# Kernel tuning notes

Hardware: AMD Instinct MI355X
Metric: run time of the kernel (lower is better)

## Reference

```python
import jax, jax.numpy as jnp
import numpy as np

EPS = 1e-8  # torch cosine_similarity default eps


def setup_inputs() -> dict:
    key = jax.random.key(0)
    x = jax.random.normal(key, (256, 200, 1024), dtype=jnp.float32)
    return {"x": x}


def reference(x):
    # x: [B, c, l]
    # Cosine-similarity Gram matrix, fused: dot(i,j) / max(||x_i||*||x_j||, eps)
    norms = jnp.linalg.norm(x, axis=-1)                      # [B, c]
    dots = jnp.einsum('bil,bjl->bij', x, x)                  # [B, c, c]
    sim = dots / jnp.maximum(norms[:, :, None] * norms[:, None, :], EPS)
    atten = jax.nn.softmax(sim, axis=-1)                     # [B, c, c]
    out = jnp.einsum('bij,bjl->bil', atten, x) + x           # bmm + residual
    return out
```

## Files before the change

kernel.cpp:

```cpp
#include <hip/hip_runtime.h>
#include <math.h>


typedef unsigned int uint32;
typedef __attribute__((ext_vector_type(8))) short bf16x8;
typedef __attribute__((ext_vector_type(4))) float f32x4;

#define CC 200
#define LL 1024
#define EPSV 1e-8f
#define PLSTR 116
#define XASTR 36
#define TSTR 116

__device__ __forceinline__ uint32 bfb(float f) {
  uint32 u = __float_as_uint(f);
  u += 0x7fffu + ((u >> 16) & 1u);
  return u >> 16;
}

__global__ __launch_bounds__(512, 1)
void spe_attn_kernel(const float* __restrict__ x, float* __restrict__ out) {
  const int tid  = threadIdx.x;
  const int lane = tid & 63;
  const int w    = tid >> 6;
  const int lm   = lane & 15;
  const int lg   = lane >> 4;
  const int bidx = blockIdx.x;
  const float* xb = x + (size_t)bidx * (CC * LL);
  float* ob       = out + (size_t)bidx * (CC * LL);

  __shared__ uint32 LDS[39312];
  uint32* pl    = LDS;
  uint32* xa0   = LDS + 24128;
  uint32* xa1   = LDS + 31616;
  uint32* xbf0  = LDS + 24128;
  uint32* xbf1  = LDS + 31616;
  float*  norms = (float*)(LDS + 39104);

  const bool two = (w < 5);
  const int rb0 = w;
  const int rb1 = two ? (w + 8) : w;

  const f32x4 fz = {0.f, 0.f, 0.f, 0.f};
  f32x4 acc[2][13];
  #pragma unroll
  for (int i = 0; i < 2; ++i)
    #pragma unroll
    for (int j = 0; j < 13; ++j) acc[i][j] = fz;

  if (tid < 288) { xa0[7200 + tid] = 0u; xa1[7200 + tid] = 0u; }

  float4 vst[7];
  #pragma unroll
  for (int i = 0; i < 7; ++i) {
    int idx = tid + i * 512;
    if (idx < 3200) {
      int row = idx >> 4, c4 = idx & 15;
      vst[i] = *(const float4*)(xb + row * LL + c4 * 4);
    }
  }
  #pragma unroll
  for (int i = 0; i < 7; ++i) {
    int idx = tid + i * 512;
    if (idx < 3200) {
      int row = idx >> 4, c4 = idx & 15;
      uint2 wv;
      wv.x = bfb(vst[i].x) | (bfb(vst[i].y) << 16);
      wv.y = bfb(vst[i].z) | (bfb(vst[i].w) << 16);
      *(uint2*)&xa0[row * XASTR + c4 * 2] = wv;
    }
  }

  for (int s = 0; s < 16; ++s) {
    __syncthreads();
    if (s + 1 < 16) {
      #pragma unroll
      for (int i = 0; i < 7; ++i) {
        int idx = tid + i * 512;
        if (idx < 3200) {
          int row = idx >> 4, c4 = idx & 15;
          vst[i] = *(const float4*)(xb + row * LL + (s + 1) * 64 + c4 * 4);
        }
      }
    }
    const uint32* cur = (s & 1) ? xa1 : xa0;
    __builtin_amdgcn_s_setprio(1);
    #pragma unroll
    for (int ks = 0; ks < 2; ++ks) {
      bf16x8 a0 = *(const bf16x8*)&cur[(rb0 * 16 + lm) * XASTR + ks * 16 + lg * 4];
      bf16x8 a1 = a0;
      if (two) a1 = *(const bf16x8*)&cur[(rb1 * 16 + lm) * XASTR + ks * 16 + lg * 4];
      #pragma unroll
      for (int ct = 0; ct < 13; ++ct) {
        bf16x8 bf = *(const bf16x8*)&cur[(ct * 16 + lm) * XASTR + ks * 16 + lg * 4];
        acc[0][ct] = __builtin_amdgcn_mfma_f32_16x16x32_bf16(a0, bf, acc[0][ct], 0, 0, 0);
        if (two)
          acc[1][ct] = __builtin_amdgcn_mfma_f32_16x16x32_bf16(a1, bf, acc[1][ct], 0, 0, 0);
      }
    }
    __builtin_amdgcn_s_setprio(0);
    if (s + 1 < 16) {
      uint32* nxt = (s & 1) ? xa0 : xa1;
      #pragma unroll
      for (int i = 0; i < 7; ++i) {
        int idx = tid + i * 512;
        if (idx < 3200) {
          int row = idx >> 4, c4 = idx & 15;
          uint2 wv;
          wv.x = bfb(vst[i].x) | (bfb(vst[i].y) << 16);
          wv.y = bfb(vst[i].z) | (bfb(vst[i].w) << 16);
          *(uint2*)&nxt[row * XASTR + c4 * 2] = wv;
        }
      }
    }
  }

  #pragma unroll
  for (int rbi = 0; rbi < 2; ++rbi) {
    if (rbi == 0 || two) {
      int rb = rbi ? rb1 : rb0;
      #pragma unroll
      for (int ct = 0; ct < 13; ++ct) {
        if (ct == rb) {
          #pragma unroll
          for (int r = 0; r < 4; ++r) {
            int ri = lg * 4 + r;
            if (lm == ri) norms[rb * 16 + ri] = sqrtf(acc[rbi][ct][r]);
          }
        }
      }
    }
  }
  __syncthreads();

  float cn[13];
  #pragma unroll
  for (int ct = 0; ct < 13; ++ct) cn[ct] = norms[ct * 16 + lm];

  #pragma unroll
  for (int rbi = 0; rbi < 2; ++rbi) {
    if (rbi == 0 || two) {
      int rb = rbi ? rb1 : rb0;
      #pragma unroll
      for (int r = 0; r < 4; ++r) {
        int grow = rb * 16 + lg * 4 + r;
        float rn = norms[grow];
        float sv[13];
        float m = -INFINITY;
        #pragma unroll
        for (int ct = 0; ct < 13; ++ct) {
          int gc = ct * 16 + lm;
          float sval = acc[rbi][ct][r] / fmaxf(rn * cn[ct], EPSV);
          sval = (gc < CC) ? sval : -INFINITY;
          sv[ct] = sval;
          m = fmaxf(m, sval);
        }
        #pragma unroll
        for (int off = 1; off < 16; off <<= 1) m = fmaxf(m, __shfl_xor(m, off));
        float sum = 0.f;
        #pragma unroll
        for (int ct = 0; ct < 13; ++ct) {
          float e = __expf(sv[ct] - m);
          sv[ct] = e;
          sum += e;
        }
        #pragma unroll
        for (int off = 1; off < 16; off <<= 1) sum += __shfl_xor(sum, off);
        float inv = 1.0f / sum;
        #pragma unroll
        for (int ct = 0; ct < 13; ++ct) {
          int gc = ct * 16 + lm;
          float p = sv[ct] * inv + ((gc == grow) ? 1.0f : 0.0f);
          uint32 pb = bfb(p);
          uint32 qb = (uint32)__shfl_xor((int)pb, 1);
          if (!(lane & 1)) pl[grow * PLSTR + ct * 8 + (lm >> 1)] = pb | (qb << 16);
        }
      }
      for (int i = lane; i < 256; i += 64) {
        int rr = i >> 4, c = i & 15;
        if (c < 12) pl[(rb * 16 + rr) * PLSTR + 100 + c] = 0u;
      }
    }
  }

  bf16x8 pa[2][7];
  #pragma unroll
  for (int ks = 0; ks < 7; ++ks) {
    pa[0][ks] = *(const bf16x8*)&pl[(rb0 * 16 + lm) * PLSTR + ks * 16 + lg * 4];
    if (two)
      pa[1][ks] = *(const bf16x8*)&pl[(rb1 * 16 + lm) * PLSTR + ks * 16 + lg * 4];
  }

  float pv[7][4];
  #pragma unroll
  for (int p = 0; p < 7; ++p) {
    int rb4 = (p * 8 + w) * 4;
    #pragma unroll
    for (int q = 0; q < 4; ++q) {
      int r = rb4 + q;
      pv[p][q] = (r < CC) ? xb[r * LL + lane] : 0.f;
    }
  }
  #pragma unroll
  for (int p = 0; p < 7; ++p) {
    int kpp = p * 8 + w;
    uint2 wv;
    wv.x = bfb(pv[p][0]) | (bfb(pv[p][1]) << 16);
    wv.y = bfb(pv[p][2]) | (bfb(pv[p][3]) << 16);
    *(uint2*)&xbf0[lane * TSTR + 2 * kpp] = wv;
  }

  for (int nc = 0; nc < 16; ++nc) {
    const int n0 = nc * 64;
    __syncthreads();
    if (nc + 1 < 16) {
      const int n1 = n0 + 64;
      #pragma unroll
      for (int p = 0; p < 7; ++p) {
        int rb4 = (p * 8 + w) * 4;
        #pragma unroll
        for (int q = 0; q < 4; ++q) {
          int r = rb4 + q;
          pv[p][q] = (r < CC) ? xb[r * LL + n1 + lane] : 0.f;
        }
      }
    }

    const uint32* XC = (nc & 1) ? xbf1 : xbf0;
    f32x4 acc2[2][4];
    #pragma unroll
    for (int i = 0; i < 2; ++i)
      #pragma unroll
      for (int j = 0; j < 4; ++j) acc2[i][j] = fz;

    __builtin_amdgcn_s_setprio(1);
    #pragma unroll
    for (int ks = 0; ks < 7; ++ks) {
      #pragma unroll
      for (int ct = 0; ct < 4; ++ct) {
        bf16x8 b = *(const bf16x8*)&XC[(ct * 16 + lm) * TSTR + ks * 16 + lg * 4];
        acc2[0][ct] = __builtin_amdgcn_mfma_f32_16x16x32_bf16(pa[0][ks], b, acc2[0][ct], 0, 0, 0);
        if (two)
          acc2[1][ct] = __builtin_amdgcn_mfma_f32_16x16x32_bf16(pa[1][ks], b, acc2[1][ct], 0, 0, 0);
      }
    }
    __builtin_amdgcn_s_setprio(0);

    if (nc + 1 < 16) {
      uint32* XN = (nc & 1) ? xbf0 : xbf1;
      #pragma unroll
      for (int p = 0; p < 7; ++p) {
        int kpp = p * 8 + w;
        uint2 wv;
        wv.x = bfb(pv[p][0]) | (bfb(pv[p][1]) << 16);
        wv.y = bfb(pv[p][2]) | (bfb(pv[p][3]) << 16);
        *(uint2*)&XN[lane * TSTR + 2 * kpp] = wv;
      }
    }

    #pragma unroll
    for (int rbi = 0; rbi < 2; ++rbi) {
      if (rbi == 0 || two) {
        int rb = rbi ? rb1 : rb0;
        #pragma unroll
        for (int ct = 0; ct < 4; ++ct) {
          #pragma unroll
          for (int r = 0; r < 4; ++r) {
            int grow = rb * 16 + lg * 4 + r;
            if (grow < CC) ob[grow * LL + n0 + ct * 16 + lm] = acc2[rbi][ct][r];
          }
        }
      }
    }
  }
}

extern "C" void kernel_launch(void* const* d_in, const int* in_sizes, int n_in,
                              void* d_out, int out_size, void* d_ws, size_t ws_size,
                              hipStream_t stream) {
  const float* x = (const float*)d_in[0];
  float* out = (float*)d_out;
  const int B = in_sizes[0] / (CC * LL);
  spe_attn_kernel<<<dim3(B), dim3(512), 0, stream>>>(x, out);
}
```

Baseline: 151.0 us.

## Use 1024-thread blocks with one row-block per wave and swizzled LDS

Result: slower. 157.4 us (+4.2%).

```diff
diff --git a/kernel.cpp b/kernel.cpp
--- a/kernel.cpp
+++ b/kernel.cpp
@@ -9,8 +9,8 @@
 #define CC 200
 #define LL 1024
 #define EPSV 1e-8f
+#define XASTR 36
 #define PLSTR 116
-#define XASTR 36
 #define TSTR 116
 
 __device__ __forceinline__ uint32 bfb(float f) {
@@ -19,7 +19,7 @@
   return u >> 16;
 }
 
-__global__ __launch_bounds__(512, 1)
+__global__ __launch_bounds__(1024, 4)
 void spe_attn_kernel(const float* __restrict__ x, float* __restrict__ out) {
   const int tid  = threadIdx.x;
   const int lane = tid & 63;
@@ -38,31 +38,25 @@
   uint32* xbf1  = LDS + 31616;
   float*  norms = (float*)(LDS + 39104);
 
-  const bool two = (w < 5);
-  const int rb0 = w;
-  const int rb1 = two ? (w + 8) : w;
-
   const f32x4 fz = {0.f, 0.f, 0.f, 0.f};
-  f32x4 acc[2][13];
-  #pragma unroll
-  for (int i = 0; i < 2; ++i)
-    #pragma unroll
-    for (int j = 0; j < 13; ++j) acc[i][j] = fz;
+  f32x4 acc[13];
+  #pragma unroll
+  for (int j = 0; j < 13; ++j) acc[j] = fz;
 
   if (tid < 288) { xa0[7200 + tid] = 0u; xa1[7200 + tid] = 0u; }
 
-  float4 vst[7];
-  #pragma unroll
-  for (int i = 0; i < 7; ++i) {
-    int idx = tid + i * 512;
+  float4 vst[4];
+  #pragma unroll
+  for (int i = 0; i < 4; ++i) {
+    int idx = tid + i * 1024;
     if (idx < 3200) {
       int row = idx >> 4, c4 = idx & 15;
       vst[i] = *(const float4*)(xb + row * LL + c4 * 4);
     }
   }
   #pragma unroll
-  for (int i = 0; i < 7; ++i) {
-    int idx = tid + i * 512;
+  for (int i = 0; i < 4; ++i) {
+    int idx = tid + i * 1024;
     if (idx < 3200) {
       int row = idx >> 4, c4 = idx & 15;
       uint2 wv;
@@ -76,8 +70,8 @@
     __syncthreads();
     if (s + 1 < 16) {
       #pragma unroll
-      for (int i = 0; i < 7; ++i) {
-        int idx = tid + i * 512;
+      for (int i = 0; i < 4; ++i) {
+        int idx = tid + i * 1024;
         if (idx < 3200) {
           int row = idx >> 4, c4 = idx & 15;
           vst[i] = *(const float4*)(xb + row * LL + (s + 1) * 64 + c4 * 4);
@@ -85,26 +79,24 @@
       }
     }
     const uint32* cur = (s & 1) ? xa1 : xa0;
-    __builtin_amdgcn_s_setprio(1);
-    #pragma unroll
-    for (int ks = 0; ks < 2; ++ks) {
-      bf16x8 a0 = *(const bf16x8*)&cur[(rb0 * 16 + lm) * XASTR + ks * 16 + lg * 4];
-      bf16x8 a1 = a0;
-      if (two) a1 = *(const bf16x8*)&cur[(rb1 * 16 + lm) * XASTR + ks * 16 + lg * 4];
-      #pragma unroll
-      for (int ct = 0; ct < 13; ++ct) {
-        bf16x8 bf = *(const bf16x8*)&cur[(ct * 16 + lm) * XASTR + ks * 16 + lg * 4];
-        acc[0][ct] = __builtin_amdgcn_mfma_f32_16x16x32_bf16(a0, bf, acc[0][ct], 0, 0, 0);
-        if (two)
-          acc[1][ct] = __builtin_amdgcn_mfma_f32_16x16x32_bf16(a1, bf, acc[1][ct], 0, 0, 0);
-      }
-    }
-    __builtin_amdgcn_s_setprio(0);
+    if (w < 13) {
+      __builtin_amdgcn_s_setprio(1);
+      #pragma unroll
+      for (int ks = 0; ks < 2; ++ks) {
+        bf16x8 a = *(const bf16x8*)&cur[(w * 16 + lm) * XASTR + ks * 16 + lg * 4];
+        #pragma unroll
+        for (int ct = 0; ct < 13; ++ct) {
+          bf16x8 b = *(const bf16x8*)&cur[(ct * 16 + lm) * XASTR + ks * 16 + lg * 4];
+          acc[ct] = __builtin_amdgcn_mfma_f32_16x16x32_bf16(a, b, acc[ct], 0, 0, 0);
+        }
+      }
+      __builtin_amdgcn_s_setprio(0);
+    }
     if (s + 1 < 16) {
       uint32* nxt = (s & 1) ? xa0 : xa1;
       #pragma unroll
-      for (int i = 0; i < 7; ++i) {
-        int idx = tid + i * 512;
+      for (int i = 0; i < 4; ++i) {
+        int idx = tid + i * 1024;
         if (idx < 3200) {
           int row = idx >> 4, c4 = idx & 15;
           uint2 wv;
@@ -116,99 +108,95 @@
     }
   }
 
-  #pragma unroll
-  for (int rbi = 0; rbi < 2; ++rbi) {
-    if (rbi == 0 || two) {
-      int rb = rbi ? rb1 : rb0;
+  if (w < 13) {
+    #pragma unroll
+    for (int ct = 0; ct < 13; ++ct) {
+      if (ct == w) {
+        #pragma unroll
+        for (int r = 0; r < 4; ++r) {
+          int ri = lg * 4 + r;
+          if (lm == ri) norms[w * 16 + ri] = sqrtf(acc[ct][r]);
+        }
+      }
+    }
+  }
+  __syncthreads();
+
+  bf16x8 pa[7];
+  if (w < 13) {
+    float cn[13];
+    #pragma unroll
+    for (int ct = 0; ct < 13; ++ct) cn[ct] = norms[ct * 16 + lm];
+
+    #pragma unroll
+    for (int r = 0; r < 4; ++r) {
+      int grow = w * 16 + lg * 4 + r;
+      float rn = norms[grow];
+      float sv[13];
+      float m = -INFINITY;
       #pragma unroll
       for (int ct = 0; ct < 13; ++ct) {
-        if (ct == rb) {
-          #pragma unroll
-          for (int r = 0; r < 4; ++r) {
-            int ri = lg * 4 + r;
-            if (lm == ri) norms[rb * 16 + ri] = sqrtf(acc[rbi][ct][r]);
-          }
-        }
-      }
-    }
-  }
-  __syncthreads();
-
-  float cn[13];
-  #pragma unroll
-  for (int ct = 0; ct < 13; ++ct) cn[ct] = norms[ct * 16 + lm];
-
-  #pragma unroll
-  for (int rbi = 0; rbi < 2; ++rbi) {
-    if (rbi == 0 || two) {
-      int rb = rbi ? rb1 : rb0;
-      #pragma unroll
-      for (int r = 0; r < 4; ++r) {
-        int grow = rb * 16 + lg * 4 + r;
-        float rn = norms[grow];
-        float sv[13];
-        float m = -INFINITY;
-        #pragma unroll
-        for (int ct = 0; ct < 13; ++ct) {
-          int gc = ct * 16 + lm;
-          float sval = acc[rbi][ct][r] / fmaxf(rn * cn[ct], EPSV);
-          sval = (gc < CC) ? sval : -INFINITY;
-          sv[ct] = sval;
-          m = fmaxf(m, sval);
-        }
-        #pragma unroll
-        for (int off = 1; off < 16; off <<= 1) m = fmaxf(m, __shfl_xor(m, off));
-        float sum = 0.f;
-        #pragma unroll
-        for (int ct = 0; ct < 13; ++ct) {
-          float e = __expf(sv[ct] - m);
-          sv[ct] = e;
-          sum += e;
-        }
-        #pragma unroll
-        for (int off = 1; off < 16; off <<= 1) sum += __shfl_xor(sum, off);
-        float inv = 1.0f / sum;
-        #pragma unroll
-        for (int ct = 0; ct < 13; ++ct) {
-          int gc = ct * 16 + lm;
-          float p = sv[ct] * inv + ((gc == grow) ? 1.0f : 0.0f);
-          uint32 pb = bfb(p);
-          uint32 qb = (uint32)__shfl_xor((int)pb, 1);
-          if (!(lane & 1)) pl[grow * PLSTR + ct * 8 + (lm >> 1)] = pb | (qb << 16);
-        }
-      }
-      for (int i = lane; i < 256; i += 64) {
-        int rr = i >> 4, c = i & 15;
-        if (c < 12) pl[(rb * 16 + rr) * PLSTR + 100 + c] = 0u;
-      }
-    }
-  }
-
-  bf16x8 pa[2][7];
-  #pragma unroll
-  for (int ks = 0; ks < 7; ++ks) {
-    pa[0][ks] = *(const bf16x8*)&pl[(rb0 * 16 + lm) * PLSTR + ks * 16 + lg * 4];
-    if (two)
-      pa[1][ks] = *(const bf16x8*)&pl[(rb1 * 16 + lm) * PLSTR + ks * 16 + lg * 4];
-  }
-
-  float pv[7][4];
-  #pragma unroll
-  for (int p = 0; p < 7; ++p) {
-    int rb4 = (p * 8 + w) * 4;
-    #pragma unroll
-    for (int q = 0; q < 4; ++q) {
-      int r = rb4 + q;
-      pv[p][q] = (r < CC) ? xb[r * LL + lane] : 0.f;
-    }
-  }
-  #pragma unroll
-  for (int p = 0; p < 7; ++p) {
-    int kpp = p * 8 + w;
-    uint2 wv;
-    wv.x = bfb(pv[p][0]) | (bfb(pv[p][1]) << 16);
-    wv.y = bfb(pv[p][2]) | (bfb(pv[p][3]) << 16);
-    *(uint2*)&xbf0[lane * TSTR + 2 * kpp] = wv;
+        int gc = ct * 16 + lm;
+        float sval = acc[ct][r] / fmaxf(rn * cn[ct], EPSV);
+        sval = (gc < CC) ? sval : -INFINITY;
+        sv[ct] = sval;
+        m = fmaxf(m, sval);
+      }
+      #pragma unroll
+      for (int off = 1; off < 16; off <<= 1) m = fmaxf(m, __shfl_xor(m, off));
+      float sum = 0.f;
+      #pragma unroll
+      for (int ct = 0; ct < 13; ++ct) {
+        float e = __expf(sv[ct] - m);
+        sv[ct] = e;
+        sum += e;
+      }
+      #pragma unroll
+      for (int off = 1; off < 16; off <<= 1) sum += __shfl_xor(sum, off);
+      float inv = 1.0f / sum;
+      #pragma unroll
+      for (int ct = 0; ct < 13; ++ct) {
+        int gc = ct * 16 + lm;
+        float p = sv[ct] * inv + ((gc == grow) ? 1.0f : 0.0f);
+        uint32 pb = bfb(p);
+        uint32 qb = (uint32)__shfl_xor((int)pb, 1);
+        if (!(lane & 1)) pl[grow * PLSTR + ct * 8 + (lm >> 1)] = pb | (qb << 16);
+      }
+    }
+    #pragma unroll
+    for (int i = 0; i < 3; ++i) {
+      int idx = lane + i * 64;
+      int rr = idx & 15, c = idx >> 4;
+      pl[(w * 16 + rr) * PLSTR + 100 + c] = 0u;
+    }
+    #pragma unroll
+    for (int ks = 0; ks < 7; ++ks)
+      pa[ks] = *(const bf16x8*)&pl[(w * 16 + lm) * PLSTR + ks * 16 + lg * 4];
+  }
+
+  float pv[4][4];
+  const int swz = ((lane >> 3) & 3) << 1;
+  #pragma unroll
+  for (int p = 0; p < 4; ++p) {
+    int kpp = p * 16 + w;
+    if (kpp < 56) {
+      int rb4 = kpp * 4;
+      #pragma unroll
+      for (int q = 0; q < 4; ++q) {
+        int r = rb4 + q;
+        pv[p][q] = (r < CC) ? xb[r * LL + lane] : 0.f;
+      }
+    }
+  }
+  #pragma unroll
+  for (int p = 0; p < 4; ++p) {
+    int kpp = p * 16 + w;
+    if (kpp < 56) {
+      uint2 wv;
+      wv.x = bfb(pv[p][0]) | (bfb(pv[p][1]) << 16);
+      wv.y = bfb(pv[p][2]) | (bfb(pv[p][3]) << 16);
+      *(uint2*)&xbf0[lane * TSTR + 2 * (kpp ^ swz)] = wv;
+    }
   }
 
   for (int nc = 0; nc < 16; ++nc) {
@@ -217,59 +205,57 @@
     if (nc + 1 < 16) {
       const int n1 = n0 + 64;
       #pragma unroll
-      for (int p = 0; p < 7; ++p) {
-        int rb4 = (p * 8 + w) * 4;
-        #pragma unroll
-        for (int q = 0; q < 4; ++q) {
-          int r = rb4 + q;
-          pv[p][q] = (r < CC) ? xb[r * LL + n1 + lane] : 0.f;
+      for (int p = 0; p < 4; ++p) {
+        int kpp = p * 16 + w;
+        if (kpp < 56) {
+          int rb4 = kpp * 4;
+          #pragma unroll
+          for (int q = 0; q < 4; ++q) {
+            int r = rb4 + q;
+            pv[p][q] = (r < CC) ? xb[r * LL + n1 + lane] : 0.f;
+          }
         }
       }
     }
 
     const uint32* XC = (nc & 1) ? xbf1 : xbf0;
-    f32x4 acc2[2][4];
-    #pragma unroll
-    for (int i = 0; i < 2; ++i)
-      #pragma unroll
-      for (int j = 0; j < 4; ++j) acc2[i][j] = fz;
-
-    __builtin_amdgcn_s_setprio(1);
-    #pragma unroll
-    for (int ks = 0; ks < 7; ++ks) {
-      #pragma unroll
-      for (int ct = 0; ct < 4; ++ct) {
-        bf16x8 b = *(const bf16x8*)&XC[(ct * 16 + lm) * TSTR + ks * 16 + lg * 4];
-        acc2[0][ct] = __builtin_amdgcn_mfma_f32_16x16x32_bf16(pa[0][ks], b, acc2[0][ct], 0, 0, 0);
-        if (two)
-          acc2[1][ct] = __builtin_amdgcn_mfma_f32_16x16x32_bf16(pa[1][ks], b, acc2[1][ct], 0, 0, 0);
-      }
-    }
-    __builtin_amdgcn_s_setprio(0);
+    f32x4 acc2[4] = {fz, fz, fz, fz};
+    if (w < 13) {
+      __builtin_amdgcn_s_setprio(1);
+      #pragma unroll
+      for (int ks = 0; ks < 7; ++ks) {
+        #pragma unroll
+        for (int ct = 0; ct < 4; ++ct) {
+          int col = ct * 16 + lm;
+          int s2 = ((col >> 3) & 3) << 1;
+          bf16x8 b = *(const bf16x8*)&XC[col * TSTR + 2 * (((ks * 8 + lg * 2)) ^ s2)];
+          acc2[ct] = __builtin_amdgcn_mfma_f32_16x16x32_bf16(pa[ks], b, acc2[ct], 0, 0, 0);
+        }
+      }
+      __builtin_amdgcn_s_setprio(0);
+    }
 
     if (nc + 1 < 16) {
       uint32* XN = (nc & 1) ? xbf0 : xbf1;
       #pragma unroll
-      for (int p = 0; p < 7; ++p) {
-        int kpp = p * 8 + w;
-        uint2 wv;
-        wv.x = bfb(pv[p][0]) | (bfb(pv[p][1]) << 16);
-        wv.y = bfb(pv[p][2]) | (bfb(pv[p][3]) << 16);
-        *(uint2*)&XN[lane * TSTR + 2 * kpp] = wv;
-      }
-    }
-
-    #pragma unroll
-    for (int rbi = 0; rbi < 2; ++rbi) {
-      if (rbi == 0 || two) {
-        int rb = rbi ? rb1 : rb0;
-        #pragma unroll
-        for (int ct = 0; ct < 4; ++ct) {
-          #pragma unroll
-          for (int r = 0; r < 4; ++r) {
-            int grow = rb * 16 + lg * 4 + r;
-            if (grow < CC) ob[grow * LL + n0 + ct * 16 + lm] = acc2[rbi][ct][r];
-          }
+      for (int p = 0; p < 4; ++p) {
+        int kpp = p * 16 + w;
+        if (kpp < 56) {
+          uint2 wv;
+          wv.x = bfb(pv[p][0]) | (bfb(pv[p][1]) << 16);
+          wv.y = bfb(pv[p][2]) | (bfb(pv[p][3]) << 16);
+          *(uint2*)&XN[lane * TSTR + 2 * (kpp ^ swz)] = wv;
+        }
+      }
+    }
+
+    if (w < 13) {
+      #pragma unroll
+      for (int ct = 0; ct < 4; ++ct) {
+        #pragma unroll
+        for (int r = 0; r < 4; ++r) {
+          int grow = w * 16 + lg * 4 + r;
+          if (grow < CC) ob[grow * LL + n0 + ct * 16 + lm] = acc2[ct][r];
         }
       }
     }
@@ -282,5 +268,5 @@
   const float* x = (const float*)d_in[0];
   float* out = (float*)d_out;
   const int B = in_sizes[0] / (CC * LL);
-  spe_attn_kernel<<<dim3(B), dim3(512), 0, stream>>>(x, out);
+  spe_attn_kernel<<<dim3(B), dim3(1024), 0, stream>>>(x, out);
 }
```

## Double K/N chunk width, drop P staging buffer, swizzle X^T LDS layout

Applied to the files above, without the earlier changes.

Result: slower. 231.0 us (+52.9%).

```diff
diff --git a/kernel.cpp b/kernel.cpp
--- a/kernel.cpp
+++ b/kernel.cpp
@@ -9,9 +9,9 @@
 #define CC 200
 #define LL 1024
 #define EPSV 1e-8f
-#define PLSTR 116
-#define XASTR 36
+#define XASTR 68
 #define TSTR 116
+#define SLOT 1856
 
 __device__ __forceinline__ uint32 bfb(float f) {
   uint32 u = __float_as_uint(f);
@@ -19,7 +19,7 @@
   return u >> 16;
 }
 
-__global__ __launch_bounds__(512, 1)
+__global__ __launch_bounds__(512, 2)
 void spe_attn_kernel(const float* __restrict__ x, float* __restrict__ out) {
   const int tid  = threadIdx.x;
   const int lane = tid & 63;
@@ -30,13 +30,12 @@
   const float* xb = x + (size_t)bidx * (CC * LL);
   float* ob       = out + (size_t)bidx * (CC * LL);
 
-  __shared__ uint32 LDS[39312];
-  uint32* pl    = LDS;
-  uint32* xa0   = LDS + 24128;
-  uint32* xa1   = LDS + 31616;
-  uint32* xbf0  = LDS + 24128;
-  uint32* xbf1  = LDS + 31616;
-  float*  norms = (float*)(LDS + 39104);
+  __shared__ uint32 LDS[29904];
+  uint32* xa0   = LDS;
+  uint32* xa1   = LDS + 14144;
+  uint32* xbf0  = LDS;
+  uint32* xbf1  = LDS + 14848;
+  float*  norms = (float*)(LDS + 29696);
 
   const bool two = (w < 5);
   const int rb0 = w;
@@ -49,22 +48,22 @@
     #pragma unroll
     for (int j = 0; j < 13; ++j) acc[i][j] = fz;
 
-  if (tid < 288) { xa0[7200 + tid] = 0u; xa1[7200 + tid] = 0u; }
-
-  float4 vst[7];
-  #pragma unroll
-  for (int i = 0; i < 7; ++i) {
+  for (int i = tid; i < 544; i += 512) { xa0[13600 + i] = 0u; xa1[13600 + i] = 0u; }
+
+  float4 vst[13];
+  #pragma unroll
+  for (int i = 0; i < 13; ++i) {
     int idx = tid + i * 512;
-    if (idx < 3200) {
-      int row = idx >> 4, c4 = idx & 15;
+    if (idx < 6400) {
+      int row = idx >> 5, c4 = idx & 31;
       vst[i] = *(const float4*)(xb + row * LL + c4 * 4);
     }
   }
   #pragma unroll
-  for (int i = 0; i < 7; ++i) {
+  for (int i = 0; i < 13; ++i) {
     int idx = tid + i * 512;
-    if (idx < 3200) {
-      int row = idx >> 4, c4 = idx & 15;
+    if (idx < 6400) {
+      int row = idx >> 5, c4 = idx & 31;
       uint2 wv;
       wv.x = bfb(vst[i].x) | (bfb(vst[i].y) << 16);
       wv.y = bfb(vst[i].z) | (bfb(vst[i].w) << 16);
@@ -72,22 +71,22 @@
     }
   }
 
-  for (int s = 0; s < 16; ++s) {
+  for (int s = 0; s < 8; ++s) {
     __syncthreads();
-    if (s + 1 < 16) {
-      #pragma unroll
-      for (int i = 0; i < 7; ++i) {
+    if (s + 1 < 8) {
+      #pragma unroll
+      for (int i = 0; i < 13; ++i) {
         int idx = tid + i * 512;
-        if (idx < 3200) {
-          int row = idx >> 4, c4 = idx & 15;
-          vst[i] = *(const float4*)(xb + row * LL + (s + 1) * 64 + c4 * 4);
+        if (idx < 6400) {
+          int row = idx >> 5, c4 = idx & 31;
+          vst[i] = *(const float4*)(xb + row * LL + (s + 1) * 128 + c4 * 4);
         }
       }
     }
     const uint32* cur = (s & 1) ? xa1 : xa0;
     __builtin_amdgcn_s_setprio(1);
     #pragma unroll
-    for (int ks = 0; ks < 2; ++ks) {
+    for (int ks = 0; ks < 4; ++ks) {
       bf16x8 a0 = *(const bf16x8*)&cur[(rb0 * 16 + lm) * XASTR + ks * 16 + lg * 4];
       bf16x8 a1 = a0;
       if (two) a1 = *(const bf16x8*)&cur[(rb1 * 16 + lm) * XASTR + ks * 16 + lg * 4];
@@ -100,13 +99,13 @@
       }
     }
     __builtin_amdgcn_s_setprio(0);
-    if (s + 1 < 16) {
+    if (s + 1 < 8) {
       uint32* nxt = (s & 1) ? xa0 : xa1;
       #pragma unroll
-      for (int i = 0; i < 7; ++i) {
+      for (int i = 0; i < 13; ++i) {
         int idx = tid + i * 512;
-        if (idx < 3200) {
-          int row = idx >> 4, c4 = idx & 15;
+        if (idx < 6400) {
+          int row = idx >> 5, c4 = idx & 31;
           uint2 wv;
           wv.x = bfb(vst[i].x) | (bfb(vst[i].y) << 16);
           wv.y = bfb(vst[i].z) | (bfb(vst[i].w) << 16);
@@ -138,13 +137,16 @@
   #pragma unroll
   for (int ct = 0; ct < 13; ++ct) cn[ct] = norms[ct * 16 + lm];
 
+  bf16x8 pa[2][7];
   #pragma unroll
   for (int rbi = 0; rbi < 2; ++rbi) {
     if (rbi == 0 || two) {
       int rb = rbi ? rb1 : rb0;
+      uint32* trp = LDS + rb * SLOT;
       #pragma unroll
       for (int r = 0; r < 4; ++r) {
         int grow = rb * 16 + lg * 4 + r;
+        int lrow = lg * 4 + r;
         float rn = norms[grow];
         float sv[13];
         float m = -INFINITY;
@@ -174,72 +176,76 @@
           float p = sv[ct] * inv + ((gc == grow) ? 1.0f : 0.0f);
           uint32 pb = bfb(p);
           uint32 qb = (uint32)__shfl_xor((int)pb, 1);
-          if (!(lane & 1)) pl[grow * PLSTR + ct * 8 + (lm >> 1)] = pb | (qb << 16);
-        }
-      }
-      for (int i = lane; i < 256; i += 64) {
-        int rr = i >> 4, c = i & 15;
-        if (c < 12) pl[(rb * 16 + rr) * PLSTR + 100 + c] = 0u;
-      }
-    }
-  }
-
-  bf16x8 pa[2][7];
-  #pragma unroll
-  for (int ks = 0; ks < 7; ++ks) {
-    pa[0][ks] = *(const bf16x8*)&pl[(rb0 * 16 + lm) * PLSTR + ks * 16 + lg * 4];
-    if (two)
-      pa[1][ks] = *(const bf16x8*)&pl[(rb1 * 16 + lm) * PLSTR + ks * 16 + lg * 4];
-  }
-
-  float pv[7][4];
-  #pragma unroll
-  for (int p = 0; p < 7; ++p) {
-    int rb4 = (p * 8 + w) * 4;
+          if (!(lane & 1)) trp[lrow * TSTR + ct * 8 + (lm >> 1)] = pb | (qb << 16);
+        }
+      }
+      #pragma unroll
+      for (int i = 0; i < 2; ++i) {
+        int idx = lane + i * 64;
+        int rr = idx >> 3, c = idx & 7;
+        trp[rr * TSTR + 104 + c] = 0u;
+      }
+      #pragma unroll
+      for (int ks = 0; ks < 7; ++ks)
+        pa[rbi][ks] = *(const bf16x8*)&trp[lm * TSTR + ks * 16 + lg * 4];
+    }
+  }
+  __syncthreads();
+
+  float pv[14][4];
+  const int swz = ((lane >> 3) & 3) << 1;
+  #pragma unroll
+  for (int p = 0; p < 14; ++p) {
+    int kpp = (p >> 1) * 8 + w;
+    int col = lane + 64 * (p & 1);
     #pragma unroll
     for (int q = 0; q < 4; ++q) {
-      int r = rb4 + q;
-      pv[p][q] = (r < CC) ? xb[r * LL + lane] : 0.f;
-    }
-  }
-  #pragma unroll
-  for (int p = 0; p < 7; ++p) {
-    int kpp = p * 8 + w;
+      int r = kpp * 4 + q;
+      pv[p][q] = (r < CC) ? xb[r * LL + col] : 0.f;
+    }
+  }
+  #pragma unroll
+  for (int p = 0; p < 14; ++p) {
+    int kpp = (p >> 1) * 8 + w;
+    int col = lane + 64 * (p & 1);
     uint2 wv;
     wv.x = bfb(pv[p][0]) | (bfb(pv[p][1]) << 16);
     wv.y = bfb(pv[p][2]) | (bfb(pv[p][3]) << 16);
-    *(uint2*)&xbf0[lane * TSTR + 2 * kpp] = wv;
-  }
-
-  for (int nc = 0; nc < 16; ++nc) {
-    const int n0 = nc * 64;
+    *(uint2*)&xbf0[col * TSTR + 2 * (kpp ^ swz)] = wv;
+  }
+
+  for (int nc = 0; nc < 8; ++nc) {
+    const int n0 = nc * 128;
     __syncthreads();
-    if (nc + 1 < 16) {
-      const int n1 = n0 + 64;
-      #pragma unroll
-      for (int p = 0; p < 7; ++p) {
-        int rb4 = (p * 8 + w) * 4;
+    if (nc + 1 < 8) {
+      const int n1 = n0 + 128;
+      #pragma unroll
+      for (int p = 0; p < 14; ++p) {
+        int kpp = (p >> 1) * 8 + w;
+        int col = lane + 64 * (p & 1);
         #pragma unroll
         for (int q = 0; q < 4; ++q) {
-          int r = rb4 + q;
-          pv[p][q] = (r < CC) ? xb[r * LL + n1 + lane] : 0.f;
+          int r = kpp * 4 + q;
+          pv[p][q] = (r < CC) ? xb[r * LL + n1 + col] : 0.f;
         }
       }
     }
 
     const uint32* XC = (nc & 1) ? xbf1 : xbf0;
-    f32x4 acc2[2][4];
+    f32x4 acc2[2][8];
     #pragma unroll
     for (int i = 0; i < 2; ++i)
       #pragma unroll
-      for (int j = 0; j < 4; ++j) acc2[i][j] = fz;
+      for (int j = 0; j < 8; ++j) acc2[i][j] = fz;
 
     __builtin_amdgcn_s_setprio(1);
     #pragma unroll
     for (int ks = 0; ks < 7; ++ks) {
       #pragma unroll
-      for (int ct = 0; ct < 4; ++ct) {
-        bf16x8 b = *(const bf16x8*)&XC[(ct * 16 + lm) * TSTR + ks * 16 + lg * 4];
+      for (int ct = 0; ct < 8; ++ct) {
+        int col = ct * 16 + lm;
+        int s2 = ((col >> 3) & 3) << 1;
+        bf16x8 b = *(const bf16x8*)&XC[col * TSTR + 2 * ((ks * 8 + lg * 2) ^ s2)];
         acc2[0][ct] = __builtin_amdgcn_mfma_f32_16x16x32_bf16(pa[0][ks], b, acc2[0][ct], 0, 0, 0);
         if (two)
           acc2[1][ct] = __builtin_amdgcn_mfma_f32_16x16x32_bf16(pa[1][ks], b, acc2[1][ct], 0, 0, 0);
@@ -247,15 +253,16 @@
     }
     __builtin_amdgcn_s_setprio(0);
 
-    if (nc + 1 < 16) {
+    if (nc + 1 < 8) {
       uint32* XN = (nc & 1) ? xbf0 : xbf1;
       #pragma unroll
-      for (int p = 0; p < 7; ++p) {
-        int kpp = p * 8 + w;
+      for (int p = 0; p < 14; ++p) {
+        int kpp = (p >> 1) * 8 + w;
+        int col = lane + 64 * (p & 1);
         uint2 wv;
         wv.x = bfb(pv[p][0]) | (bfb(pv[p][1]) << 16);
         wv.y = bfb(pv[p][2]) | (bfb(pv[p][3]) << 16);
-        *(uint2*)&XN[lane * TSTR + 2 * kpp] = wv;
+        *(uint2*)&XN[col * TSTR + 2 * (kpp ^ swz)] = wv;
       }
     }
 
@@ -264,7 +271,7 @@
       if (rbi == 0 || two) {
         int rb = rbi ? rb1 : rb0;
         #pragma unroll
-        for (int ct = 0; ct < 4; ++ct) {
+        for (int ct = 0; ct < 8; ++ct) {
           #pragma unroll
           for (int r = 0; r < 4; ++r) {
             int grow = rb * 16 + lg * 4 + r;
```
